# Kernel optimization log

Hardware: AMD Instinct MI355X
Metric: run time of the kernel (lower is better)

Reference implementation:

```python
import jax, jax.numpy as jnp
import numpy as np

N_HEAD = 16
HEAD_DIM = 64  # n_embd // n_head = 1024 // 16


def setup_inputs() -> dict:
    key = jax.random.key(0)
    ks = jax.random.split(key, 4)
    B, T, C = 4, 2048, 1024
    x = jax.random.normal(ks[0], (B, T, C), dtype=jnp.float32)
    W_qkv = jax.random.normal(ks[1], (C, 3 * C), dtype=jnp.float32) * (1.0 / np.sqrt(C))
    b_qkv = jnp.zeros((3 * C,), dtype=jnp.float32)
    W_proj = jax.random.normal(ks[2], (C, C), dtype=jnp.float32) * (1.0 / np.sqrt(C))
    b_proj = jnp.zeros((C,), dtype=jnp.float32)
    return {"x": x, "W_qkv": W_qkv, "b_qkv": b_qkv, "W_proj": W_proj, "b_proj": b_proj}


def reference(x, W_qkv, b_qkv, W_proj, b_proj):
    B, T, C = x.shape
    H, D = N_HEAD, HEAD_DIM
    qkv = x @ W_qkv + b_qkv                      # [B, T, 3C]
    qkv = qkv.reshape(B, T, 3, H, D)
    q = jnp.transpose(qkv[:, :, 0], (0, 2, 1, 3))  # [B, H, T, D]
    k = jnp.transpose(qkv[:, :, 1], (0, 2, 1, 3))
    v = jnp.transpose(qkv[:, :, 2], (0, 2, 1, 3))
    scale = 1.0 / np.sqrt(D).astype(np.float32)
    att = jnp.einsum('bhqd,bhkd->bhqk', q, k) * scale  # [B, H, T, T]
    causal = jnp.tril(jnp.ones((T, T), dtype=bool))
    att = jnp.where(causal[None, None], att, -jnp.inf)
    att = jax.nn.softmax(att, axis=-1)
    # dropout p=0.0 (eval / identity)
    y = jnp.einsum('bhqk,bhkd->bhqd', att, v)  # [B, H, T, D]
    y = jnp.transpose(y, (0, 2, 1, 3)).reshape(B, T, C)
    return y @ W_proj + b_proj
```

## Files before the change

### kernel.cpp

```cpp
#include <hip/hip_runtime.h>
#include <hip/hip_bf16.h>

#define TT 2048
#define CCH 1024
#define HH 16
#define DD 64
#define BB 4
#define MM (BB*TT)

typedef __attribute__((ext_vector_type(4))) float f32x4;
typedef __attribute__((ext_vector_type(8))) short short8;
typedef __attribute__((ext_vector_type(8))) unsigned short u16x8;
typedef __attribute__((ext_vector_type(4))) unsigned short u16x4;

__device__ __forceinline__ unsigned short f2b(float f) {
    unsigned int u = __float_as_uint(f);
    u += 0x7fffu + ((u >> 16) & 1u);
    return (unsigned short)(u >> 16);
}
__device__ __forceinline__ float b2f(unsigned short u) {
    return __uint_as_float(((unsigned int)u) << 16);
}
__device__ __forceinline__ int finite_f(float v) {
    return ((__float_as_uint(v) >> 23) & 0xFFu) != 0xFFu;
}
__device__ __forceinline__ float exp2_hw(float x) {
    return __builtin_amdgcn_exp2f(x);
}

__global__ __launch_bounds__(64) void detect_k(const unsigned int* __restrict__ x,
                                               int* __restrict__ flag) {
    int tid = threadIdx.x;
    int cnt = 0;
#pragma unroll
    for (int i = 0; i < 16; ++i) {
        unsigned int w = x[tid * 16 + i];
        unsigned int lo = w & 0xFFFFu;
        unsigned int e = (lo >> 7) & 0xFFu;
        if ((e >= 0x62u && e <= 0x90u) || lo == 0u) ++cnt;
    }
#pragma unroll
    for (int o = 32; o; o >>= 1) cnt += __shfl_down(cnt, o);
    if (tid == 0) *flag = (cnt >= 640) ? 1 : 0;
}

__global__ __launch_bounds__(256) void wtrans_k(const void* __restrict__ in,
                                                unsigned short* __restrict__ out,
                                                int R, int Cc,
                                                const int* __restrict__ flag) {
    __shared__ float tile[32][33];
    const int tid = threadIdx.x;
    const int c0 = blockIdx.x * 32, r0 = blockIdx.y * 32;
    const int isb = *flag;
#pragma unroll
    for (int i = 0; i < 4; ++i) {
        int e = i * 256 + tid;
        int row = e >> 5, col = e & 31;
        size_t idx = (size_t)(r0 + row) * Cc + (c0 + col);
        tile[row][col] = isb ? b2f(((const unsigned short*)in)[idx])
                             : ((const float*)in)[idx];
    }
    __syncthreads();
#pragma unroll
    for (int i = 0; i < 4; ++i) {
        int e = i * 256 + tid;
        int crow = e >> 5, rcol = e & 31;
        out[(size_t)(c0 + crow) * R + (r0 + rcol)] = f2b(tile[rcol][crow]);
    }
}

__global__ __launch_bounds__(256) void vtrans_k(const unsigned short* __restrict__ V,
                                                unsigned short* __restrict__ VT) {
    __shared__ unsigned short tile[64][68];
    const int tid = threadIdx.x;
    const int t0 = blockIdx.x * 64;
    const int bh = blockIdx.y;
    const unsigned short* in = V + ((size_t)bh * TT + t0) * DD;
#pragma unroll
    for (int i = 0; i < 4; ++i) {
        int cid = i * 256 + tid;
        int row = cid >> 4;
        int ch  = cid & 15;
        u16x4 v = *(const u16x4*)(in + row * DD + ch * 4);
        *(u16x4*)&tile[row][ch * 4] = v;
    }
    __syncthreads();
    unsigned short* out = VT + (size_t)bh * DD * TT + t0;
#pragma unroll
    for (int i = 0; i < 4; ++i) {
        int cid = i * 256 + tid;
        int drow = cid >> 4;
        int tch  = cid & 15;
        u16x4 v;
        v[0] = tile[tch * 4 + 0][drow];
        v[1] = tile[tch * 4 + 1][drow];
        v[2] = tile[tch * 4 + 2][drow];
        v[3] = tile[tch * 4 + 3][drow];
        *(u16x4*)(out + (size_t)drow * TT + tch * 4) = v;
    }
}

__global__ __launch_bounds__(256) void gemm_qkv(const void* __restrict__ x,
                                                const unsigned short* __restrict__ Bt,
                                                const void* __restrict__ bias,
                                                unsigned short* __restrict__ outQ,
                                                unsigned short* __restrict__ outK,
                                                unsigned short* __restrict__ outV,
                                                const int* __restrict__ flag) {
    __shared__ unsigned short As[128 * 32];
    __shared__ unsigned short Bs[128 * 32];
    const int Ksz = CCH;
    const int tid = threadIdx.x;
    const int lane = tid & 63;
    const int wid = tid >> 6;
    const int bm = blockIdx.y * 128;
    const int bn = blockIdx.x * 128;
    const int wm = (wid >> 1) * 64;
    const int wn = (wid & 1) * 64;
    const int sr = tid >> 2;
    const int sc = (tid & 3) * 8;
    const int l15 = lane & 15, l4 = lane >> 4;
    const int isb = *flag;

    f32x4 acc[4][4];
#pragma unroll
    for (int i = 0; i < 4; ++i)
#pragma unroll
        for (int j = 0; j < 4; ++j)
            acc[i][j] = (f32x4){0.f, 0.f, 0.f, 0.f};

    const size_t aoff0 = (size_t)(bm + sr) * Ksz + sc;
    const size_t aoff1 = aoff0 + (size_t)64 * Ksz;
    const unsigned short* pb0 = Bt + (size_t)(bn + sr) * Ksz + sc;
    const unsigned short* pb1 = pb0 + (size_t)64 * Ksz;

    auto lda = [&](size_t off) -> u16x8 {
        if (isb) return *(const u16x8*)((const unsigned short*)x + off);
        const float4* p = (const float4*)((const float*)x + off);
        float4 v0 = p[0], v1 = p[1];
        u16x8 o;
        o[0] = f2b(v0.x); o[1] = f2b(v0.y); o[2] = f2b(v0.z); o[3] = f2b(v0.w);
        o[4] = f2b(v1.x); o[5] = f2b(v1.y); o[6] = f2b(v1.z); o[7] = f2b(v1.w);
        return o;
    };

    u16x8 a0 = lda(aoff0);
    u16x8 a1 = lda(aoff1);
    u16x8 b0 = *(const u16x8*)(pb0);
    u16x8 b1 = *(const u16x8*)(pb1);

    for (int kt = 0; kt < Ksz; kt += 32) {
        __syncthreads();
        *(u16x8*)&As[sr * 32 + sc] = a0;
        *(u16x8*)&As[(sr + 64) * 32 + sc] = a1;
        *(u16x8*)&Bs[sr * 32 + sc] = b0;
        *(u16x8*)&Bs[(sr + 64) * 32 + sc] = b1;
        if (kt + 32 < Ksz) {
            a0 = lda(aoff0 + kt + 32);
            a1 = lda(aoff1 + kt + 32);
            b0 = *(const u16x8*)(pb0 + kt + 32);
            b1 = *(const u16x8*)(pb1 + kt + 32);
        }
        __syncthreads();
        short8 af[4], bfr[4];
#pragma unroll
        for (int mi = 0; mi < 4; ++mi)
            af[mi] = *(const short8*)&As[(wm + mi * 16 + l15) * 32 + l4 * 8];
#pragma unroll
        for (int ni = 0; ni < 4; ++ni)
            bfr[ni] = *(const short8*)&Bs[(wn + ni * 16 + l15) * 32 + l4 * 8];
#pragma unroll
        for (int mi = 0; mi < 4; ++mi)
#pragma unroll
            for (int ni = 0; ni < 4; ++ni)
                acc[mi][ni] = __builtin_amdgcn_mfma_f32_16x16x32_bf16(
                    af[mi], bfr[ni], acc[mi][ni], 0, 0, 0);
    }

#pragma unroll
    for (int mi = 0; mi < 4; ++mi) {
#pragma unroll
        for (int ni = 0; ni < 4; ++ni) {
            const int col = bn + wn + ni * 16 + l15;
            const float bv = isb ? b2f(((const unsigned short*)bias)[col])
                                 : ((const float*)bias)[col];
#pragma unroll
            for (int r = 0; r < 4; ++r) {
                const int row = bm + wm + mi * 16 + l4 * 4 + r;
                float v = acc[mi][ni][r] + bv;
                const int which = col >> 10;
                const int h = (col >> 6) & 15;
                const int d = col & 63;
                const int b = row >> 11, t = row & 2047;
                const size_t idx = (((size_t)b * HH + h) * TT + t) * DD + d;
                if (which == 0)      outQ[idx] = f2b(v * 0.18033688f);
                else if (which == 1) outK[idx] = f2b(v);
                else                 outV[idx] = f2b(v);
            }
        }
    }
}

__global__ __launch_bounds__(256) void attn_k(unsigned short* __restrict__ Q,
                                              const unsigned short* __restrict__ K,
                                              const unsigned short* __restrict__ VT) {
    __shared__ __align__(16) char shmem[32000];
    const int tid = threadIdx.x, lane = tid & 63, h = tid >> 6;
    const int bid = blockIdx.x;
    const int swb = (bid & 7) * 256 + (bid >> 3);
    const int bh = swb >> 5;
    const int pair = swb & 31;
    const int l15 = lane & 15, l4 = lane >> 4;
    unsigned short* Qp = Q + (size_t)bh * TT * DD;
    const unsigned short* Kp = K + (size_t)bh * TT * DD;
    const unsigned short* Vp = VT + (size_t)bh * DD * TT;
    const int swz = (l15 & 7) << 4;
    unsigned short (*PldsW)[64] = (unsigned short (*)[64])(shmem + h * 4096);
    unsigned char* prowA = (unsigned char*)&PldsW[l15][0];
    unsigned char* prowB = (unsigned char*)&PldsW[16 + l15][0];
    float* MrgF = (float*)shmem;
    unsigned short (*Olds)[34] = (unsigned short (*)[34])(shmem + 27648);

#pragma unroll 1
    for (int hv = 0; hv < 2; ++hv) {
        const int qt = hv ? (63 - pair) : pair;
        const int qw = qt << 5;
        const int qiA = qw + l15, qiB = qw + 16 + l15;
        const int kend = qw + 32;

        short8 qfA0 = *(const short8*)(Qp + (size_t)(qw + l15) * DD + l4 * 8);
        short8 qfA1 = *(const short8*)(Qp + (size_t)(qw + l15) * DD + 32 + l4 * 8);
        short8 qfB0 = *(const short8*)(Qp + (size_t)(qw + 16 + l15) * DD + l4 * 8);
        short8 qfB1 = *(const short8*)(Qp + (size_t)(qw + 16 + l15) * DD + 32 + l4 * 8);

        f32x4 otA[4], otB[4];
#pragma unroll
        for (int c = 0; c < 4; ++c) {
            otA[c] = (f32x4){0.f, 0.f, 0.f, 0.f};
            otB[c] = (f32x4){0.f, 0.f, 0.f, 0.f};
        }
        float mA = -1e30f, lA = 0.f, mB = -1e30f, lB = 0.f;

        auto softmax16 = [&](f32x4 (&st)[4], float& m, float& lsum, f32x4 (&ot)[4],
                             int qi, bool needMask, int kb, unsigned char* prow) {
            if (needMask) {
#pragma unroll
                for (int t = 0; t < 4; ++t)
#pragma unroll
                    for (int r = 0; r < 4; ++r) {
                        const int kpos = kb + t * 16 + l4 * 4 + r;
                        st[t][r] = (kpos > qi) ? -30000.f : st[t][r];
                    }
            }
            float mx0 = fmaxf(fmaxf(st[0][0], st[0][1]), fmaxf(st[0][2], st[0][3]));
            float mx1 = fmaxf(fmaxf(st[1][0], st[1][1]), fmaxf(st[1][2], st[1][3]));
            float mx2 = fmaxf(fmaxf(st[2][0], st[2][1]), fmaxf(st[2][2], st[2][3]));
            float mx3 = fmaxf(fmaxf(st[3][0], st[3][1]), fmaxf(st[3][2], st[3][3]));
            float tmax = fmaxf(fmaxf(mx0, mx1), fmaxf(mx2, mx3));
            tmax = fmaxf(tmax, __shfl_xor(tmax, 16));
            tmax = fmaxf(tmax, __shfl_xor(tmax, 32));
            if (!__all(tmax <= m + 8.f)) {
                const float mnew = fmaxf(m, tmax);
                const float corr = exp2_hw(m - mnew);
                lsum *= corr;
#pragma unroll
                for (int c = 0; c < 4; ++c) ot[c] *= corr;
                m = mnew;
            }
            u16x4 pw[4];
            float s0 = 0.f, s1 = 0.f, s2 = 0.f, s3 = 0.f;
#pragma unroll
            for (int t = 0; t < 4; ++t)
#pragma unroll
                for (int r = 0; r < 4; ++r) {
                    float p = exp2_hw(st[t][r] - m);
                    if (t == 0) s0 += p; else if (t == 1) s1 += p;
                    else if (t == 2) s2 += p; else s3 += p;
                    pw[t][r] = f2b(p);
                }
            lsum += (s0 + s1) + (s2 + s3);
#pragma unroll
            for (int t = 0; t < 4; ++t)
                *(u16x4*)(prow + ((t * 32 + l4 * 8) ^ swz)) = pw[t];
        };

#pragma unroll 1
        for (int kb = h * 64; kb < kend; kb += 256) {
            short8 kf[4][2];
#pragma unroll
            for (int t = 0; t < 4; ++t) {
                const unsigned short* kr = Kp + (size_t)(kb + t * 16 + l15) * DD + l4 * 8;
                kf[t][0] = *(const short8*)(kr);
                kf[t][1] = *(const short8*)(kr + 32);
            }
            short8 vf[4][2];
#pragma unroll
            for (int c = 0; c < 4; ++c)
#pragma unroll
                for (int ch = 0; ch < 2; ++ch)
                    vf[c][ch] = *(const short8*)(Vp + (size_t)(c * 16 + l15) * TT
                                                 + kb + ch * 32 + l4 * 8);
            f32x4 st[4];
            __builtin_amdgcn_s_setprio(1);
#pragma unroll
            for (int t = 0; t < 4; ++t) {
                f32x4 z = (f32x4){0.f, 0.f, 0.f, 0.f};
                z = __builtin_amdgcn_mfma_f32_16x16x32_bf16(kf[t][0], qfA0, z, 0, 0, 0);
                z = __builtin_amdgcn_mfma_f32_16x16x32_bf16(kf[t][1], qfA1, z, 0, 0, 0);
                st[t] = z;
            }
            __builtin_amdgcn_s_setprio(0);
            softmax16(st, mA, lA, otA, qiA, kb + 63 > qw, kb, prowA);
            __builtin_amdgcn_s_setprio(1);
#pragma unroll
            for (int t = 0; t < 4; ++t) {
                f32x4 z = (f32x4){0.f, 0.f, 0.f, 0.f};
                z = __builtin_amdgcn_mfma_f32_16x16x32_bf16(kf[t][0], qfB0, z, 0, 0, 0);
                z = __builtin_amdgcn_mfma_f32_16x16x32_bf16(kf[t][1], qfB1, z, 0, 0, 0);
                st[t] = z;
            }
            __builtin_amdgcn_s_setprio(0);
            softmax16(st, mB, lB, otB, qiB, kb + 63 > qw + 16, kb, prowB);
            asm volatile("" ::: "memory");
            short8 pbA0 = *(const short8*)(prowA + ((l4 * 16) ^ swz));
            short8 pbA1 = *(const short8*)(prowA + ((64 + l4 * 16) ^ swz));
            short8 pbB0 = *(const short8*)(prowB + ((l4 * 16) ^ swz));
            short8 pbB1 = *(const short8*)(prowB + ((64 + l4 * 16) ^ swz));
            asm volatile("" ::: "memory");
            __builtin_amdgcn_s_setprio(1);
#pragma unroll
            for (int c = 0; c < 4; ++c) {
                otA[c] = __builtin_amdgcn_mfma_f32_16x16x32_bf16(vf[c][0], pbA0, otA[c], 0, 0, 0);
                otA[c] = __builtin_amdgcn_mfma_f32_16x16x32_bf16(vf[c][1], pbA1, otA[c], 0, 0, 0);
                otB[c] = __builtin_amdgcn_mfma_f32_16x16x32_bf16(vf[c][0], pbB0, otB[c], 0, 0, 0);
                otB[c] = __builtin_amdgcn_mfma_f32_16x16x32_bf16(vf[c][1], pbB1, otB[c], 0, 0, 0);
            }
            __builtin_amdgcn_s_setprio(0);
        }

        float lsA = lA + __shfl_xor(lA, 16);
        lsA += __shfl_xor(lsA, 32);
        float lsB = lB + __shfl_xor(lB, 16);
        lsB += __shfl_xor(lsB, 32);

        __syncthreads();
        if (h > 0) {
            float* mb = MrgF + ((size_t)(h - 1) * 64 + lane) * 36;
            mb[0] = mA; mb[1] = lsA; mb[2] = mB; mb[3] = lsB;
#pragma unroll
            for (int c = 0; c < 4; ++c)
#pragma unroll
                for (int r = 0; r < 4; ++r) {
                    mb[4 + c * 4 + r]  = otA[c][r];
                    mb[20 + c * 4 + r] = otB[c][r];
                }
        }
        __syncthreads();
        if (h == 0) {
            auto merge16 = [&](float m0, float ls0, const f32x4 (&ot)[4],
                               int mOff, int oOff, int col) {
                float mj[3], lj[3];
                float mstar = m0;
#pragma unroll
                for (int j = 0; j < 3; ++j) {
                    mj[j] = MrgF[((size_t)j * 64 + lane) * 36 + mOff];
                    lj[j] = MrgF[((size_t)j * 64 + lane) * 36 + mOff + 1];
                    mstar = fmaxf(mstar, mj[j]);
                }
                const float cs = exp2_hw(m0 - mstar);
                float cj[3];
                float den = ls0 * cs;
#pragma unroll
                for (int j = 0; j < 3; ++j) {
                    cj[j] = exp2_hw(mj[j] - mstar);
                    den += lj[j] * cj[j];
                }
                const float inv = 1.f / den;
#pragma unroll
                for (int c = 0; c < 4; ++c)
#pragma unroll
                    for (int r = 0; r < 4; ++r) {
                        float v = ot[c][r] * cs;
#pragma unroll
                        for (int j = 0; j < 3; ++j)
                            v += MrgF[((size_t)j * 64 + lane) * 36 + oOff + c * 4 + r] * cj[j];
                        v *= inv;
                        if (!finite_f(v)) v = 200.0f;
                        Olds[c * 16 + l4 * 4 + r][col] = f2b(v);
                    }
            };
            merge16(mA, lsA, otA, 0, 4, l15);
            merge16(mB, lsB, otB, 2, 20, 16 + l15);
            asm volatile("" ::: "memory");
            const int qr = lane >> 1, hf = lane & 1;
#pragma unroll
            for (int chunk = 0; chunk < 4; ++chunk) {
                u16x8 o;
#pragma unroll
                for (int j = 0; j < 8; ++j) o[j] = Olds[hf * 32 + chunk * 8 + j][qr];
                *(u16x8*)(Qp + (size_t)(qw + qr) * DD + hf * 32 + chunk * 8) = o;
            }
        }
        __syncthreads();
    }
}

__global__ __launch_bounds__(256) void gemm_proj(const unsigned short* __restrict__ A,
                                                 const unsigned short* __restrict__ Bt,
                                                 const void* __restrict__ bias,
                                                 float* __restrict__ outO,
                                                 const int* __restrict__ flag) {
    __shared__ unsigned short As[128 * 32];
    __shared__ unsigned short Bs[128 * 32];
    const int Ksz = CCH;
    const int tid = threadIdx.x;
    const int lane = tid & 63;
    const int wid = tid >> 6;
    const int bm = blockIdx.y * 128;
    const int bn = blockIdx.x * 128;
    const int wm = (wid >> 1) * 64;
    const int wn = (wid & 1) * 64;
    const int sr = tid >> 2;
    const int sc = (tid & 3) * 8;
    const int l15 = lane & 15, l4 = lane >> 4;
    const int isb = *flag;

    f32x4 acc[4][4];
#pragma unroll
    for (int i = 0; i < 4; ++i)
#pragma unroll
        for (int j = 0; j < 4; ++j)
            acc[i][j] = (f32x4){0.f, 0.f, 0.f, 0.f};

    const int m0 = bm + sr;
    const unsigned short* Ar0 = A + (size_t)(m0 >> 11) * (HH * TT * DD)
                                  + (size_t)(m0 & 2047) * DD;
    const unsigned short* Ar1 = Ar0 + (size_t)64 * DD;
    const unsigned short* pb0 = Bt + (size_t)(bn + sr) * Ksz + sc;
    const unsigned short* pb1 = pb0 + (size_t)64 * Ksz;

    auto aoff = [&](int kt) -> size_t {
        return (size_t)(kt >> 6) * (TT * DD) + (kt & 32) + sc;
    };

    u16x8 a0 = *(const u16x8*)(Ar0 + aoff(0));
    u16x8 a1 = *(const u16x8*)(Ar1 + aoff(0));
    u16x8 b0 = *(const u16x8*)(pb0);
    u16x8 b1 = *(const u16x8*)(pb1);

    for (int kt = 0; kt < Ksz; kt += 32) {
        __syncthreads();
        *(u16x8*)&As[sr * 32 + sc] = a0;
        *(u16x8*)&As[(sr + 64) * 32 + sc] = a1;
        *(u16x8*)&Bs[sr * 32 + sc] = b0;
        *(u16x8*)&Bs[(sr + 64) * 32 + sc] = b1;
        if (kt + 32 < Ksz) {
            a0 = *(const u16x8*)(Ar0 + aoff(kt + 32));
            a1 = *(const u16x8*)(Ar1 + aoff(kt + 32));
            b0 = *(const u16x8*)(pb0 + kt + 32);
            b1 = *(const u16x8*)(pb1 + kt + 32);
        }
        __syncthreads();
        short8 af[4], bfr[4];
#pragma unroll
        for (int mi = 0; mi < 4; ++mi)
            af[mi] = *(const short8*)&As[(wm + mi * 16 + l15) * 32 + l4 * 8];
#pragma unroll
        for (int ni = 0; ni < 4; ++ni)
            bfr[ni] = *(const short8*)&Bs[(wn + ni * 16 + l15) * 32 + l4 * 8];
#pragma unroll
        for (int mi = 0; mi < 4; ++mi)
#pragma unroll
            for (int ni = 0; ni < 4; ++ni)
                acc[mi][ni] = __builtin_amdgcn_mfma_f32_16x16x32_bf16(
                    af[mi], bfr[ni], acc[mi][ni], 0, 0, 0);
    }

#pragma unroll
    for (int mi = 0; mi < 4; ++mi) {
#pragma unroll
        for (int ni = 0; ni < 4; ++ni) {
            const int col = bn + wn + ni * 16 + l15;
            const float bv = isb ? b2f(((const unsigned short*)bias)[col])
                                 : ((const float*)bias)[col];
#pragma unroll
            for (int r = 0; r < 4; ++r) {
                const int row = bm + wm + mi * 16 + l4 * 4 + r;
                float v = acc[mi][ni][r] + bv;
                if (!finite_f(v)) v = 300.0f;
                outO[(size_t)row * CCH + col] = v;
            }
        }
    }
}

extern "C" void kernel_launch(void* const* d_in, const int* in_sizes, int n_in,
                              void* d_out, int out_size, void* d_ws, size_t ws_size,
                              hipStream_t stream) {
    const void* x     = d_in[0];
    const void* Wqkv  = d_in[1];
    const void* bqkv  = d_in[2];
    const void* Wproj = d_in[3];
    const void* bproj = d_in[4];
    float* out = (float*)d_out;

    char* w = (char*)d_ws;
    int* flag = (int*)w;                          w += 256;
    unsigned short* wqkvT  = (unsigned short*)w;  w += (size_t)3 * CCH * CCH * 2;
    unsigned short* wprojT = (unsigned short*)w;  w += (size_t)CCH * CCH * 2;
    unsigned short* Qb     = (unsigned short*)w;  w += (size_t)MM * CCH * 2;
    unsigned short* Kb     = (unsigned short*)w;  w += (size_t)MM * CCH * 2;
    unsigned short* VTb    = (unsigned short*)w;  w += (size_t)MM * CCH * 2;
    unsigned short* Vstage = (unsigned short*)d_out;

    detect_k<<<1, 64, 0, stream>>>((const unsigned int*)x, flag);
    wtrans_k<<<dim3(96, 32), 256, 0, stream>>>(Wqkv, wqkvT, CCH, 3 * CCH, flag);
    wtrans_k<<<dim3(32, 32), 256, 0, stream>>>(Wproj, wprojT, CCH, CCH, flag);
    gemm_qkv<<<dim3(24, 64), 256, 0, stream>>>(x, wqkvT, bqkv, Qb, Kb, Vstage, flag);
    vtrans_k<<<dim3(32, 64), 256, 0, stream>>>(Vstage, VTb);
    attn_k<<<2048, 256, 0, stream>>>(Qb, Kb, VTb);
    gemm_proj<<<dim3(8, 64), 256, 0, stream>>>(Qb, wprojT, bproj, out, flag);
}
```

Baseline: 297.9 us.

## Pre-cast x to bf16 and use direct global-to-LDS loads in GEMMs

Adds a separate kernel that casts x to bf16 into the output buffer, so the QKV GEMM no longer converts fp32 to bf16 inside its load loop. Both GEMMs now fill shared memory with global_load_lds (direct global-to-LDS DMA) instead of staging the data through registers. This frees registers and VALU work, but it drops the register prefetch: each k-step now issues its loads and waits on them within a single barrier pair, with no overlap of loads and compute. The cast also adds an extra pass over x through memory.

```diff
diff --git a/kernel.cpp b/kernel.cpp
--- a/kernel.cpp
+++ b/kernel.cpp
@@ -28,6 +28,12 @@
     return __builtin_amdgcn_exp2f(x);
 }
 
+typedef const __attribute__((address_space(1))) unsigned int g_u32;
+typedef __attribute__((address_space(3))) unsigned int l_u32;
+__device__ __forceinline__ void gl_lds16(const unsigned short* g, unsigned short* l) {
+    __builtin_amdgcn_global_load_lds((g_u32*)g, (l_u32*)l, 16, 0, 0);
+}
+
 __global__ __launch_bounds__(64) void detect_k(const unsigned int* __restrict__ x,
                                                int* __restrict__ flag) {
     int tid = threadIdx.x;
@@ -42,6 +48,23 @@
 #pragma unroll
     for (int o = 32; o; o >>= 1) cnt += __shfl_down(cnt, o);
     if (tid == 0) *flag = (cnt >= 640) ? 1 : 0;
+}
+
+__global__ __launch_bounds__(256) void cast_x_k(const void* __restrict__ in,
+                                                unsigned short* __restrict__ out,
+                                                const int* __restrict__ flag) {
+    int g = blockIdx.x * 256 + threadIdx.x;
+    if (*flag) {
+        *(u16x8*)(out + (size_t)g * 8) =
+            *(const u16x8*)((const unsigned short*)in + (size_t)g * 8);
+    } else {
+        const float4* p = (const float4*)((const float*)in + (size_t)g * 8);
+        float4 v0 = p[0], v1 = p[1];
+        u16x8 o;
+        o[0] = f2b(v0.x); o[1] = f2b(v0.y); o[2] = f2b(v0.z); o[3] = f2b(v0.w);
+        o[4] = f2b(v1.x); o[5] = f2b(v1.y); o[6] = f2b(v1.z); o[7] = f2b(v1.w);
+        *(u16x8*)(out + (size_t)g * 8) = o;
+    }
 }
 
 __global__ __launch_bounds__(256) void wtrans_k(const void* __restrict__ in,
@@ -100,7 +123,7 @@
     }
 }
 
-__global__ __launch_bounds__(256) void gemm_qkv(const void* __restrict__ x,
+__global__ __launch_bounds__(256) void gemm_qkv(const unsigned short* __restrict__ A,
                                                 const unsigned short* __restrict__ Bt,
                                                 const void* __restrict__ bias,
                                                 unsigned short* __restrict__ outQ,
@@ -129,38 +152,21 @@
         for (int j = 0; j < 4; ++j)
             acc[i][j] = (f32x4){0.f, 0.f, 0.f, 0.f};
 
-    const size_t aoff0 = (size_t)(bm + sr) * Ksz + sc;
-    const size_t aoff1 = aoff0 + (size_t)64 * Ksz;
+    const unsigned short* pa0 = A + (size_t)(bm + sr) * Ksz + sc;
+    const unsigned short* pa1 = pa0 + (size_t)64 * Ksz;
     const unsigned short* pb0 = Bt + (size_t)(bn + sr) * Ksz + sc;
     const unsigned short* pb1 = pb0 + (size_t)64 * Ksz;
-
-    auto lda = [&](size_t off) -> u16x8 {
-        if (isb) return *(const u16x8*)((const unsigned short*)x + off);
-        const float4* p = (const float4*)((const float*)x + off);
-        float4 v0 = p[0], v1 = p[1];
-        u16x8 o;
-        o[0] = f2b(v0.x); o[1] = f2b(v0.y); o[2] = f2b(v0.z); o[3] = f2b(v0.w);
-        o[4] = f2b(v1.x); o[5] = f2b(v1.y); o[6] = f2b(v1.z); o[7] = f2b(v1.w);
-        return o;
-    };
-
-    u16x8 a0 = lda(aoff0);
-    u16x8 a1 = lda(aoff1);
-    u16x8 b0 = *(const u16x8*)(pb0);
-    u16x8 b1 = *(const u16x8*)(pb1);
+    unsigned short* lA0 = &As[sr * 32 + sc];
+    unsigned short* lA1 = &As[(sr + 64) * 32 + sc];
+    unsigned short* lB0 = &Bs[sr * 32 + sc];
+    unsigned short* lB1 = &Bs[(sr + 64) * 32 + sc];
 
     for (int kt = 0; kt < Ksz; kt += 32) {
         __syncthreads();
-        *(u16x8*)&As[sr * 32 + sc] = a0;
-        *(u16x8*)&As[(sr + 64) * 32 + sc] = a1;
-        *(u16x8*)&Bs[sr * 32 + sc] = b0;
-        *(u16x8*)&Bs[(sr + 64) * 32 + sc] = b1;
-        if (kt + 32 < Ksz) {
-            a0 = lda(aoff0 + kt + 32);
-            a1 = lda(aoff1 + kt + 32);
-            b0 = *(const u16x8*)(pb0 + kt + 32);
-            b1 = *(const u16x8*)(pb1 + kt + 32);
-        }
+        gl_lds16(pa0 + kt, lA0);
+        gl_lds16(pa1 + kt, lA1);
+        gl_lds16(pb0 + kt, lB0);
+        gl_lds16(pb1 + kt, lB1);
         __syncthreads();
         short8 af[4], bfr[4];
 #pragma unroll
@@ -438,28 +444,21 @@
     const unsigned short* Ar1 = Ar0 + (size_t)64 * DD;
     const unsigned short* pb0 = Bt + (size_t)(bn + sr) * Ksz + sc;
     const unsigned short* pb1 = pb0 + (size_t)64 * Ksz;
+    unsigned short* lA0 = &As[sr * 32 + sc];
+    unsigned short* lA1 = &As[(sr + 64) * 32 + sc];
+    unsigned short* lB0 = &Bs[sr * 32 + sc];
+    unsigned short* lB1 = &Bs[(sr + 64) * 32 + sc];
 
     auto aoff = [&](int kt) -> size_t {
         return (size_t)(kt >> 6) * (TT * DD) + (kt & 32) + sc;
     };
 
-    u16x8 a0 = *(const u16x8*)(Ar0 + aoff(0));
-    u16x8 a1 = *(const u16x8*)(Ar1 + aoff(0));
-    u16x8 b0 = *(const u16x8*)(pb0);
-    u16x8 b1 = *(const u16x8*)(pb1);
-
     for (int kt = 0; kt < Ksz; kt += 32) {
         __syncthreads();
-        *(u16x8*)&As[sr * 32 + sc] = a0;
-        *(u16x8*)&As[(sr + 64) * 32 + sc] = a1;
-        *(u16x8*)&Bs[sr * 32 + sc] = b0;
-        *(u16x8*)&Bs[(sr + 64) * 32 + sc] = b1;
-        if (kt + 32 < Ksz) {
-            a0 = *(const u16x8*)(Ar0 + aoff(kt + 32));
-            a1 = *(const u16x8*)(Ar1 + aoff(kt + 32));
-            b0 = *(const u16x8*)(pb0 + kt + 32);
-            b1 = *(const u16x8*)(pb1 + kt + 32);
-        }
+        gl_lds16(Ar0 + aoff(kt), lA0);
+        gl_lds16(Ar1 + aoff(kt), lA1);
+        gl_lds16(pb0 + kt, lB0);
+        gl_lds16(pb1 + kt, lB1);
         __syncthreads();
         short8 af[4], bfr[4];
 #pragma unroll
@@ -511,12 +510,14 @@
     unsigned short* Qb     = (unsigned short*)w;  w += (size_t)MM * CCH * 2;
     unsigned short* Kb     = (unsigned short*)w;  w += (size_t)MM * CCH * 2;
     unsigned short* VTb    = (unsigned short*)w;  w += (size_t)MM * CCH * 2;
-    unsigned short* Vstage = (unsigned short*)d_out;
+    unsigned short* xb     = (unsigned short*)d_out;
+    unsigned short* Vstage = (unsigned short*)d_out + (size_t)MM * CCH;
 
     detect_k<<<1, 64, 0, stream>>>((const unsigned int*)x, flag);
+    cast_x_k<<<MM * CCH / 8 / 256, 256, 0, stream>>>(x, xb, flag);
     wtrans_k<<<dim3(96, 32), 256, 0, stream>>>(Wqkv, wqkvT, CCH, 3 * CCH, flag);
     wtrans_k<<<dim3(32, 32), 256, 0, stream>>>(Wproj, wprojT, CCH, CCH, flag);
-    gemm_qkv<<<dim3(24, 64), 256, 0, stream>>>(x, wqkvT, bqkv, Qb, Kb, Vstage, flag);
+    gemm_qkv<<<dim3(24, 64), 256, 0, stream>>>(xb, wqkvT, bqkv, Qb, Kb, Vstage, flag);
     vtrans_k<<<dim3(32, 64), 256, 0, stream>>>(Vstage, VTb);
     attn_k<<<2048, 256, 0, stream>>>(Qb, Kb, VTb);
     gemm_proj<<<dim3(8, 64), 256, 0, stream>>>(Qb, wprojT, bproj, out, flag);
```

New measurement: 278.8 us. 1.07x faster.
